# Kernel tuning notes

Hardware: AMD Instinct MI355X
Metric: run time of the kernel (lower is better)

## Reference

```python
import jax, jax.numpy as jnp
import numpy as np

B, N, T, C = 16, 12, 128, 128  # batch, num_classes (nodes), temporal, channels


def _bn(x, gamma, beta, eps=1e-5):
    # BatchNorm2d in training mode: stats over (batch, t, c), channel axis 1, biased var
    mean = jnp.mean(x, axis=(0, 2, 3), keepdims=True)
    var = jnp.var(x, axis=(0, 2, 3), keepdims=True)
    xn = (x - mean) * jax.lax.rsqrt(var + eps)
    return xn * gamma[None, :, None, None] + beta[None, :, None, None]


def setup_inputs() -> dict:
    key = jax.random.key(0)
    ks = jax.random.split(key, 3)
    scale = np.float32(np.sqrt(2.0 / C))
    inp = {
        'x': jax.random.normal(ks[0], (B, N, T, C), dtype=jnp.float32),
        'edge': jax.random.normal(ks[1], (B, N * N, T, C), dtype=jnp.float32),
    }
    wk = jax.random.split(ks[2], 10)
    for name, k in zip(['A1', 'B1', 'E1', 'U1', 'V1', 'A2', 'B2', 'E2', 'U2', 'V2'], wk):
        inp[name] = jax.random.normal(k, (C, C), dtype=jnp.float32) * scale
    for name, dim in [('g_e1', N * N), ('b_e1', N * N), ('g_v1', N), ('b_v1', N),
                      ('g_e2', N * N), ('b_e2', N * N), ('g_v2', N), ('b_v2', N)]:
        inp[name] = jnp.ones((dim,), jnp.float32) if name[0] == 'g' else jnp.zeros((dim,), jnp.float32)
    return inp


def _forward(x, edge, A1, B1, E1, U1, V1, A2, B2, E2, U2, V2,
             g_e1, b_e1, g_v1, b_v1, g_e2, b_e2, g_v2, b_v2):
    # create_e_matrix: edge index e = i*N + j; 'end' selects node i, 'start' selects node j.
    # Dense incidence einsums become pure gathers; the transpose einsum is a
    # scatter-add over j, i.e. a reshape + sum.
    i_idx = jnp.repeat(jnp.arange(N), N)  # end-node of each edge
    j_idx = jnp.tile(jnp.arange(N), N)    # start-node of each edge
    b, _, t, c = x.shape

    def layer(x, edge, A, Bw, E, U, V, ge, be, gv, bv, mask_node):
        res = x
        edge_upd = (x @ A.T)[:, i_idx] + (x @ Bw.T)[:, j_idx] + edge @ E.T
        edge_upd = _bn(edge_upd, ge, be)
        edge_upd = jnp.where(jnp.isnan(edge_upd), 0.0, edge_upd)
        edge = edge + jax.nn.relu(edge_upd)
        e = jax.nn.sigmoid(edge)
        e = jax.nn.softmax(e.reshape(b, N, N, t, c), axis=2).reshape(b, N * N, t, c)
        Ujx = (x @ V.T)[:, j_idx]
        agg = (e * Ujx).reshape(b, N, N, t, c).sum(axis=2) / N  # scatter to end nodes
        xn = _bn(x @ U.T + agg, gv, bv)
        if mask_node:  # original only NaN-masks node BN in layer 1
            xn = jnp.where(jnp.isnan(xn), 0.0, xn)
        return jax.nn.relu(res + xn), edge

    x, edge = layer(x, edge, A1, B1, E1, U1, V1, g_e1, b_e1, g_v1, b_v1, True)
    x, edge = layer(x, edge, A2, B2, E2, U2, V2, g_e2, b_e2, g_v2, b_v2, False)
    return x, edge


def reference(x, edge, A1, B1, E1, U1, V1, A2, B2, E2, U2, V2,
              g_e1, b_e1, g_v1, b_v1, g_e2, b_e2, g_v2, b_v2):
    return _forward(x, edge, A1, B1, E1, U1, V1, A2, B2, E2, U2, V2,
                    g_e1, b_e1, g_v1, b_v1, g_e2, b_e2, g_v2, b_v2)
```

## Files before the change

kernel.cpp:

```cpp
#include <hip/hip_runtime.h>
#include <hip/hip_bf16.h>

#define BB 16
#define NN 12
#define NE 144
#define TT 128
#define CC 128

typedef __attribute__((ext_vector_type(8))) short v8s;
typedef __attribute__((ext_vector_type(4))) short v4s;
typedef __attribute__((ext_vector_type(4))) float v4f;

__device__ __forceinline__ short f2bf(float f) {
    unsigned u = __float_as_uint(f);
    u += 0x7fffu + ((u >> 16) & 1u);
    return (short)(u >> 16);
}
__device__ __forceinline__ float bf2f(unsigned short u) {
    return __uint_as_float(((unsigned)u) << 16);
}
__device__ __forceinline__ float rndbf(float f) { return bf2f((unsigned short)f2bf(f)); }
__device__ __forceinline__ v4s f4_to_bf4(float4 a) {
    v4s r; r[0] = f2bf(a.x); r[1] = f2bf(a.y); r[2] = f2bf(a.z); r[3] = f2bf(a.w); return r;
}

__global__ __launch_bounds__(256) void kW(
    const float* A1, const float* B1, const float* E1, const float* U1, const float* V1,
    const float* A2, const float* B2, const float* E2, const float* U2, const float* V2,
    unsigned short* wb)
{
    int idx = blockIdx.x * 256 + threadIdx.x;
    int w = idx >> 14, r = idx & 16383;
    const float* s;
    switch (w) {
        case 0: s = A1; break; case 1: s = B1; break; case 2: s = E1; break;
        case 3: s = U1; break; case 4: s = V1; break; case 5: s = A2; break;
        case 6: s = B2; break; case 7: s = E2; break; case 8: s = U2; break;
        default: s = V2; break;
    }
    wb[idx] = (unsigned short)f2bf(s[r]);
}

__global__ __launch_bounds__(256) void kP(
    const float* __restrict__ x, const unsigned short* __restrict__ wb,
    int sA, int sB, int sV, int sU,
    unsigned short* __restrict__ oA, unsigned short* __restrict__ oB,
    unsigned short* __restrict__ oV, unsigned short* __restrict__ oU)
{
    __shared__ unsigned short xt[64][136];
    int tid = threadIdx.x;
    int m0 = blockIdx.x * 64;
    #pragma unroll
    for (int it = 0; it < 8; ++it) {
        int f = it * 256 + tid;
        int row = f >> 5, c4 = f & 31;
        float4 v = *reinterpret_cast<const float4*>(x + (size_t)m0 * 128 + (size_t)f * 4);
        *reinterpret_cast<v4s*>(&xt[row][c4 * 4]) = f4_to_bf4(v);
    }
    __syncthreads();
    int lane = tid & 63, wid = tid >> 6;
    int l15 = lane & 15, l4 = lane >> 4;

    const unsigned short* Ws[4] = { wb + (size_t)sA * 16384, wb + (size_t)sB * 16384,
                                    wb + (size_t)sV * 16384, wb + (size_t)sU * 16384 };
    unsigned short* Os[4] = { oA, oB, oV, oU };

    #pragma unroll
    for (int w = 0; w < 4; ++w) {
        const unsigned short* W = Ws[w];
        unsigned short* out = Os[w];
        v8s bfr[2][4];
        #pragma unroll
        for (int nt2 = 0; nt2 < 2; ++nt2) {
            int col = (wid * 2 + nt2) * 16 + l15;
            #pragma unroll
            for (int kk = 0; kk < 4; ++kk)
                bfr[nt2][kk] = *reinterpret_cast<const v8s*>(W + col * 128 + kk * 32 + l4 * 8);
        }
        v4f acc[4][2] = {};
        #pragma unroll
        for (int kk = 0; kk < 4; ++kk) {
            #pragma unroll
            for (int mt = 0; mt < 4; ++mt) {
                v8s a = *reinterpret_cast<const v8s*>(&xt[mt * 16 + l15][kk * 32 + l4 * 8]);
                acc[mt][0] = __builtin_amdgcn_mfma_f32_16x16x32_bf16(a, bfr[0][kk], acc[mt][0], 0, 0, 0);
                acc[mt][1] = __builtin_amdgcn_mfma_f32_16x16x32_bf16(a, bfr[1][kk], acc[mt][1], 0, 0, 0);
            }
        }
        #pragma unroll
        for (int mt = 0; mt < 4; ++mt) {
            #pragma unroll
            for (int nt2 = 0; nt2 < 2; ++nt2) {
                int col = (wid * 2 + nt2) * 16 + l15;
                #pragma unroll
                for (int reg = 0; reg < 4; ++reg) {
                    int rowg = m0 + mt * 16 + l4 * 4 + reg;
                    out[(size_t)rowg * 128 + col] = (unsigned short)f2bf(acc[mt][nt2][reg]);
                }
            }
        }
    }
}

template<bool IN_F32>
__global__ __launch_bounds__(256, 4) void kA(
    const float* __restrict__ ef32, const unsigned short* __restrict__ ebf_in,
    unsigned short* __restrict__ ebf_out,
    const unsigned short* __restrict__ xAp, const unsigned short* __restrict__ xBp,
    const unsigned short* __restrict__ Ebf, float2* __restrict__ epart)
{
    __shared__ unsigned short et[64][136];
    __shared__ float sblk[2];
    int tid = threadIdx.x;
    int bid = blockIdx.x;
    int th = bid & 1; int m = bid >> 1;
    int e = m % NE, b = m / NE;
    int iA = e / 12, jA = e - iA * 12;
    int t0 = th * 64;
    if (tid < 2) sblk[tid] = 0.f;
    size_t erow0 = ((size_t)(b * NE + e) * TT + t0) * CC;

    if constexpr (IN_F32) {
        #pragma unroll
        for (int it = 0; it < 8; ++it) {
            int f = it * 256 + tid;
            int row = f >> 5, c4 = f & 31;
            float4 v = *reinterpret_cast<const float4*>(ef32 + erow0 + (size_t)row * CC + c4 * 4);
            v4s bv = f4_to_bf4(v);
            *reinterpret_cast<v4s*>(&et[row][c4 * 4]) = bv;
            *reinterpret_cast<v4s*>(ebf_out + erow0 + (size_t)row * CC + c4 * 4) = bv;
        }
    } else {
        #pragma unroll
        for (int it = 0; it < 4; ++it) {
            int f = it * 256 + tid;
            int row = f >> 4, c8 = f & 15;
            *reinterpret_cast<v8s*>(&et[row][c8 * 8]) =
                *reinterpret_cast<const v8s*>(ebf_in + erow0 + (size_t)row * CC + c8 * 8);
        }
    }
    __syncthreads();

    int lane = tid & 63, wid = tid >> 6;
    int l15 = lane & 15, l4 = lane >> 4;

    v8s bfr[2][4];
    #pragma unroll
    for (int nt2 = 0; nt2 < 2; ++nt2) {
        int col = (wid * 2 + nt2) * 16 + l15;
        #pragma unroll
        for (int kk = 0; kk < 4; ++kk)
            bfr[nt2][kk] = *reinterpret_cast<const v8s*>(Ebf + col * 128 + kk * 32 + l4 * 8);
    }
    v4f acc[4][2] = {};
    #pragma unroll
    for (int kk = 0; kk < 4; ++kk) {
        #pragma unroll
        for (int mt = 0; mt < 4; ++mt) {
            v8s a = *reinterpret_cast<const v8s*>(&et[mt * 16 + l15][kk * 32 + l4 * 8]);
            acc[mt][0] = __builtin_amdgcn_mfma_f32_16x16x32_bf16(a, bfr[0][kk], acc[mt][0], 0, 0, 0);
            acc[mt][1] = __builtin_amdgcn_mfma_f32_16x16x32_bf16(a, bfr[1][kk], acc[mt][1], 0, 0, 0);
        }
    }
    __syncthreads();
    #pragma unroll
    for (int mt = 0; mt < 4; ++mt) {
        #pragma unroll
        for (int nt2 = 0; nt2 < 2; ++nt2) {
            int col = (wid * 2 + nt2) * 16 + l15;
            #pragma unroll
            for (int reg = 0; reg < 4; ++reg)
                et[mt * 16 + l4 * 4 + reg][col] = (unsigned short)f2bf(acc[mt][nt2][reg]);
        }
    }
    __syncthreads();
    size_t xaoff = ((size_t)(b * NN + iA) * TT + t0) * CC;
    size_t xboff = ((size_t)(b * NN + jA) * TT + t0) * CC;
    float s = 0.f, q = 0.f;
    #pragma unroll
    for (int it = 0; it < 4; ++it) {
        int f = it * 256 + tid;
        int row = f >> 4, c8 = f & 15;
        v8s ev = *reinterpret_cast<const v8s*>(&et[row][c8 * 8]);
        v8s xa = *reinterpret_cast<const v8s*>(xAp + xaoff + (size_t)row * CC + c8 * 8);
        v8s xb = *reinterpret_cast<const v8s*>(xBp + xboff + (size_t)row * CC + c8 * 8);
        #pragma unroll
        for (int k = 0; k < 8; ++k) {
            float v = bf2f((unsigned short)ev[k]) + bf2f((unsigned short)xa[k])
                    + bf2f((unsigned short)xb[k]);
            s += v; q += v * v;
        }
    }
    #pragma unroll
    for (int off = 1; off < 64; off <<= 1) { s += __shfl_xor(s, off); q += __shfl_xor(q, off); }
    if (lane == 0) { atomicAdd(&sblk[0], s); atomicAdd(&sblk[1], q); }
    __syncthreads();
    if (tid == 0) epart[bid] = make_float2(sblk[0], sblk[1]);
}

__global__ __launch_bounds__(64) void kRede(
    const float2* __restrict__ epart, const float* __restrict__ g,
    const float* __restrict__ be, float* __restrict__ estats)
{
    int e = blockIdx.x;
    int tid = threadIdx.x;
    float s = 0.f, q = 0.f;
    if (tid < 32) {
        int b = tid >> 1, th = tid & 1;
        float2 p = epart[(size_t)(b * NE + e) * 2 + th];
        s = p.x; q = p.y;
    }
    #pragma unroll
    for (int off = 1; off < 32; off <<= 1) { s += __shfl_xor(s, off); q += __shfl_xor(q, off); }
    if (tid == 0) {
        const float M = 262144.f;
        float mean = s / M;
        float var = q / M - mean * mean;
        float sc = g[e] * rsqrtf(var + 1e-5f);
        estats[e * 2] = sc;
        estats[e * 2 + 1] = be[e] - mean * sc;
    }
}

template<bool OUT_F32>
__global__ __launch_bounds__(256, 4) void kC(
    unsigned short* __restrict__ ebf,
    float* __restrict__ eout,
    const unsigned short* __restrict__ xAp, const unsigned short* __restrict__ xBp,
    const unsigned short* __restrict__ xV, const unsigned short* __restrict__ xU,
    const unsigned short* __restrict__ Ebf, const float* __restrict__ estats,
    unsigned short* __restrict__ yout, float* __restrict__ npart)
{
    __shared__ unsigned short et[48][136];
    __shared__ unsigned short xab[16][136];
    __shared__ unsigned short xv[12][136];
    __shared__ float2 scf[48];
    __shared__ float ns[4], nq[4];
    int tid = threadIdx.x;
    int bid = blockIdx.x;
    int third = bid % 3; int bt = bid / 3;
    int b = bt >> 7, t = bt & 127;
    if (tid < 48) scf[tid] = make_float2(estats[(third * 48 + tid) * 2],
                                         estats[(third * 48 + tid) * 2 + 1]);
    if (tid < 4) { ns[tid] = 0.f; nq[tid] = 0.f; }
    {
        int row = tid >> 4, c8 = tid & 15;
        const unsigned short* src = (row < 4)
            ? (xAp + (((size_t)(b * NN + third * 4 + row) * TT) + t) * CC)
            : (xBp + (((size_t)(b * NN + (row - 4)) * TT) + t) * CC);
        *reinterpret_cast<v8s*>(&xab[row][c8 * 8]) = *reinterpret_cast<const v8s*>(src + c8 * 8);
    }
    if (tid < 192) {
        int row = tid >> 4, c8 = tid & 15;
        *reinterpret_cast<v8s*>(&xv[row][c8 * 8]) =
            *reinterpret_cast<const v8s*>(xV + (((size_t)(b * NN + row) * TT) + t) * CC + c8 * 8);
    }
    #pragma unroll
    for (int it = 0; it < 3; ++it) {
        int f = it * 256 + tid;
        int row = f >> 4, c8 = f & 15;
        *reinterpret_cast<v8s*>(&et[row][c8 * 8]) =
            *reinterpret_cast<const v8s*>(ebf + (((size_t)(b * NE + third * 48 + row) * TT) + t) * CC + c8 * 8);
    }
    __syncthreads();
    int lane = tid & 63, wid = tid >> 6;
    int l15 = lane & 15, l4 = lane >> 4;

    v8s bfr[2][4];
    #pragma unroll
    for (int nt2 = 0; nt2 < 2; ++nt2) {
        int col = (wid * 2 + nt2) * 16 + l15;
        #pragma unroll
        for (int kk = 0; kk < 4; ++kk)
            bfr[nt2][kk] = *reinterpret_cast<const v8s*>(Ebf + col * 128 + kk * 32 + l4 * 8);
    }
    v4f acc[3][2] = {};
    #pragma unroll
    for (int kk = 0; kk < 4; ++kk) {
        #pragma unroll
        for (int mt = 0; mt < 3; ++mt) {
            v8s a = *reinterpret_cast<const v8s*>(&et[mt * 16 + l15][kk * 32 + l4 * 8]);
            acc[mt][0] = __builtin_amdgcn_mfma_f32_16x16x32_bf16(a, bfr[0][kk], acc[mt][0], 0, 0, 0);
            acc[mt][1] = __builtin_amdgcn_mfma_f32_16x16x32_bf16(a, bfr[1][kk], acc[mt][1], 0, 0, 0);
        }
    }
    __syncthreads();
    #pragma unroll
    for (int mt = 0; mt < 3; ++mt) {
        #pragma unroll
        for (int reg = 0; reg < 4; ++reg) {
            int r = mt * 16 + l4 * 4 + reg;
            int il = r / 12, jl = r - il * 12;
            float2 sc = scf[r];
            #pragma unroll
            for (int nt2 = 0; nt2 < 2; ++nt2) {
                int col = (wid * 2 + nt2) * 16 + l15;
                float upd = rndbf(acc[mt][nt2][reg]) + bf2f(xab[il][col]) + bf2f(xab[4 + jl][col]);
                float bn = fmaxf(sc.x * upd + sc.y, 0.f);
                float en = bf2f(et[r][col]) + bn;
                et[r][col] = (unsigned short)f2bf(en);
                if constexpr (OUT_F32) {
                    int eg = third * 48 + r;
                    eout[(((size_t)(b * NE + eg) * TT) + t) * CC + col] = en;
                }
            }
        }
    }
    __syncthreads();
    if constexpr (!OUT_F32) {
        #pragma unroll
        for (int it = 0; it < 3; ++it) {
            int f = it * 256 + tid;
            int row = f >> 4, c8 = f & 15;
            *reinterpret_cast<v8s*>(ebf + (((size_t)(b * NE + third * 48 + row) * TT) + t) * CC + c8 * 8) =
                *reinterpret_cast<const v8s*>(&et[row][c8 * 8]);
        }
    }
    #pragma unroll
    for (int ph = 0; ph < 2; ++ph) {
        int u = tid + ph * 256;
        int il = u >> 7, c = u & 127;
        float den = 0.f, ag = 0.f;
        #pragma unroll
        for (int j = 0; j < 12; ++j) {
            float sv = bf2f(et[il * 12 + j][c]);
            float sg = 1.f / (1.f + __expf(-sv));
            float ev = __expf(sg);
            den += ev;
            ag += ev * bf2f(xv[j][c]);
        }
        float agg = ag / (den * 12.f);
        int i = third * 4 + il;
        size_t xa = (((size_t)(b * NN + i) * TT) + t) * CC + c;
        float yv = bf2f(xU[xa]) + agg;
        unsigned short us = (unsigned short)f2bf(yv);
        yout[xa] = us;
        float yr = bf2f(us);
        float s1 = yr, s2 = yr * yr;
        #pragma unroll
        for (int off = 1; off < 64; off <<= 1) { s1 += __shfl_xor(s1, off); s2 += __shfl_xor(s2, off); }
        if (lane == 0) { atomicAdd(&ns[il], s1); atomicAdd(&nq[il], s2); }
    }
    __syncthreads();
    if (tid < 4) {
        npart[(size_t)bid * 8 + tid * 2 + 0] = ns[tid];
        npart[(size_t)bid * 8 + tid * 2 + 1] = nq[tid];
    }
}

__global__ __launch_bounds__(256) void kRedn(
    const float* __restrict__ npart, const float* __restrict__ g,
    const float* __restrict__ be, float* __restrict__ nstats)
{
    int n = blockIdx.x;
    int third = n >> 2, il = n & 3;
    float s = 0.f, q = 0.f;
    for (int bt = threadIdx.x; bt < 2048; bt += 256) {
        const float* p = npart + ((size_t)(bt * 3 + third) * 8 + il * 2);
        s += p[0]; q += p[1];
    }
    __shared__ float ss[4], qq[4];
    #pragma unroll
    for (int off = 32; off >= 1; off >>= 1) { s += __shfl_down(s, off); q += __shfl_down(q, off); }
    int wid = threadIdx.x >> 6;
    if ((threadIdx.x & 63) == 0) { ss[wid] = s; qq[wid] = q; }
    __syncthreads();
    if (threadIdx.x == 0) {
        s = ss[0] + ss[1] + ss[2] + ss[3];
        q = qq[0] + qq[1] + qq[2] + qq[3];
        const float M = 262144.f;
        float mean = s / M;
        float var = q / M - mean * mean;
        float sc = g[n] * rsqrtf(var + 1e-5f);
        nstats[n * 2] = sc;
        nstats[n * 2 + 1] = be[n] - mean * sc;
    }
}

__global__ __launch_bounds__(256) void kE(
    const float* xres, const unsigned short* __restrict__ yin,
    const float* __restrict__ nstats, float* xout)
{
    int idx4 = blockIdx.x * 256 + threadIdx.x;
    size_t base = (size_t)idx4 * 4;
    int n = (int)((base >> 14) % 12);
    float scv = nstats[n * 2], shv = nstats[n * 2 + 1];
    float4 xvv = *reinterpret_cast<const float4*>(xres + base);
    v4s yv4 = *reinterpret_cast<const v4s*>(yin + base);
    float4 o;
    o.x = fmaxf(xvv.x + scv * bf2f((unsigned short)yv4[0]) + shv, 0.f);
    o.y = fmaxf(xvv.y + scv * bf2f((unsigned short)yv4[1]) + shv, 0.f);
    o.z = fmaxf(xvv.z + scv * bf2f((unsigned short)yv4[2]) + shv, 0.f);
    o.w = fmaxf(xvv.w + scv * bf2f((unsigned short)yv4[3]) + shv, 0.f);
    *reinterpret_cast<float4*>(xout + base) = o;
}

extern "C" void kernel_launch(void* const* d_in, const int* in_sizes, int n_in,
                              void* d_out, int out_size, void* d_ws, size_t ws_size,
                              hipStream_t stream)
{
    const float* x0 = (const float*)d_in[0];
    const float* e0 = (const float*)d_in[1];
    const float* W[10];
    for (int i = 0; i < 10; ++i) W[i] = (const float*)d_in[2 + i];
    const float* ge1 = (const float*)d_in[12];
    const float* be1 = (const float*)d_in[13];
    const float* gv1 = (const float*)d_in[14];
    const float* bv1 = (const float*)d_in[15];
    const float* ge2 = (const float*)d_in[16];
    const float* be2 = (const float*)d_in[17];
    const float* gv2 = (const float*)d_in[18];
    const float* bv2 = (const float*)d_in[19];

    const size_t SZX = (size_t)BB * NN * TT * CC;
    const size_t SZE = (size_t)BB * NE * TT * CC;
    float* out_x = (float*)d_out;
    float* out_e = out_x + SZX;

    unsigned short* ws16 = (unsigned short*)d_ws;
    unsigned short* xA = ws16;
    unsigned short* xB = ws16 + SZX;
    unsigned short* xV = ws16 + 2 * SZX;
    unsigned short* xU = ws16 + 3 * SZX;
    unsigned short* yb = ws16 + 4 * SZX;
    unsigned short* ebf = ws16 + 5 * SZX;
    float2* epart  = (float2*)(ebf + SZE);
    float* estats = (float*)(epart + 4608);
    float* npart  = estats + 288;
    float* nstats = npart + 49152;
    unsigned short* wb = (unsigned short*)(nstats + 24);

    float* x1 = out_x;

    kW<<<640, 256, 0, stream>>>(W[0], W[1], W[2], W[3], W[4], W[5], W[6], W[7], W[8], W[9], wb);

    kP<<<384, 256, 0, stream>>>(x0, wb, 0, 1, 4, 3, xA, xB, xV, xU);
    kA<true><<<4608, 256, 0, stream>>>(e0, nullptr, ebf, xA, xB, wb + 2 * 16384, epart);
    kRede<<<144, 64, 0, stream>>>(epart, ge1, be1, estats);
    kC<false><<<6144, 256, 0, stream>>>(ebf, nullptr, xA, xB, xV, xU,
                                        wb + 2 * 16384, estats, yb, npart);
    kRedn<<<12, 256, 0, stream>>>(npart, gv1, bv1, nstats);
    kE<<<3072, 256, 0, stream>>>(x0, yb, nstats, x1);

    kP<<<384, 256, 0, stream>>>(x1, wb, 5, 6, 9, 8, xA, xB, xV, xU);
    kA<false><<<4608, 256, 0, stream>>>(nullptr, ebf, nullptr, xA, xB, wb + 7 * 16384, epart);
    kRede<<<144, 64, 0, stream>>>(epart, ge2, be2, estats);
    kC<true><<<6144, 256, 0, stream>>>(ebf, out_e, xA, xB, xV, xU,
                                       wb + 7 * 16384, estats, yb, npart);
    kRedn<<<12, 256, 0, stream>>>(npart, gv2, bv2, nstats);
    kE<<<3072, 256, 0, stream>>>(x1, yb, nstats, out_x);
}
```

Measured before the change: 274.9 us.

## Split kA into quarter-time tiles and fold edge BN stats reduction into kC

kA now handles 32 time steps per block instead of 64, which doubles the grid and raises the occupancy hint. The separate kRede kernel is removed. Each kC block instead reduces the per-block partial sums for its 48 edges and builds the BN scale and shift itself. The f32 edge output in kC is also written with coalesced vectorized float4 stores from shared memory instead of scattered scalar stores. The cost is redundant stats reduction across the 6144 kC blocks (each reads 64 partials per edge), in exchange for one fewer launch per layer.

```diff
diff --git a/kernel.cpp b/kernel.cpp
--- a/kernel.cpp
+++ b/kernel.cpp
@@ -103,26 +103,26 @@
 }
 
 template<bool IN_F32>
-__global__ __launch_bounds__(256, 4) void kA(
+__global__ __launch_bounds__(256, 6) void kA(
     const float* __restrict__ ef32, const unsigned short* __restrict__ ebf_in,
     unsigned short* __restrict__ ebf_out,
     const unsigned short* __restrict__ xAp, const unsigned short* __restrict__ xBp,
     const unsigned short* __restrict__ Ebf, float2* __restrict__ epart)
 {
-    __shared__ unsigned short et[64][136];
+    __shared__ unsigned short et[32][136];
     __shared__ float sblk[2];
     int tid = threadIdx.x;
     int bid = blockIdx.x;
-    int th = bid & 1; int m = bid >> 1;
+    int th = bid & 3; int m = bid >> 2;
     int e = m % NE, b = m / NE;
     int iA = e / 12, jA = e - iA * 12;
-    int t0 = th * 64;
+    int t0 = th * 32;
     if (tid < 2) sblk[tid] = 0.f;
     size_t erow0 = ((size_t)(b * NE + e) * TT + t0) * CC;
 
     if constexpr (IN_F32) {
         #pragma unroll
-        for (int it = 0; it < 8; ++it) {
+        for (int it = 0; it < 4; ++it) {
             int f = it * 256 + tid;
             int row = f >> 5, c4 = f & 31;
             float4 v = *reinterpret_cast<const float4*>(ef32 + erow0 + (size_t)row * CC + c4 * 4);
@@ -132,7 +132,7 @@
         }
     } else {
         #pragma unroll
-        for (int it = 0; it < 4; ++it) {
+        for (int it = 0; it < 2; ++it) {
             int f = it * 256 + tid;
             int row = f >> 4, c8 = f & 15;
             *reinterpret_cast<v8s*>(&et[row][c8 * 8]) =
@@ -152,11 +152,11 @@
         for (int kk = 0; kk < 4; ++kk)
             bfr[nt2][kk] = *reinterpret_cast<const v8s*>(Ebf + col * 128 + kk * 32 + l4 * 8);
     }
-    v4f acc[4][2] = {};
+    v4f acc[2][2] = {};
     #pragma unroll
     for (int kk = 0; kk < 4; ++kk) {
         #pragma unroll
-        for (int mt = 0; mt < 4; ++mt) {
+        for (int mt = 0; mt < 2; ++mt) {
             v8s a = *reinterpret_cast<const v8s*>(&et[mt * 16 + l15][kk * 32 + l4 * 8]);
             acc[mt][0] = __builtin_amdgcn_mfma_f32_16x16x32_bf16(a, bfr[0][kk], acc[mt][0], 0, 0, 0);
             acc[mt][1] = __builtin_amdgcn_mfma_f32_16x16x32_bf16(a, bfr[1][kk], acc[mt][1], 0, 0, 0);
@@ -164,7 +164,7 @@
     }
     __syncthreads();
     #pragma unroll
-    for (int mt = 0; mt < 4; ++mt) {
+    for (int mt = 0; mt < 2; ++mt) {
         #pragma unroll
         for (int nt2 = 0; nt2 < 2; ++nt2) {
             int col = (wid * 2 + nt2) * 16 + l15;
@@ -178,7 +178,7 @@
     size_t xboff = ((size_t)(b * NN + jA) * TT + t0) * CC;
     float s = 0.f, q = 0.f;
     #pragma unroll
-    for (int it = 0; it < 4; ++it) {
+    for (int it = 0; it < 2; ++it) {
         int f = it * 256 + tid;
         int row = f >> 4, c8 = f & 15;
         v8s ev = *reinterpret_cast<const v8s*>(&et[row][c8 * 8]);
@@ -198,37 +198,15 @@
     if (tid == 0) epart[bid] = make_float2(sblk[0], sblk[1]);
 }
 
-__global__ __launch_bounds__(64) void kRede(
-    const float2* __restrict__ epart, const float* __restrict__ g,
-    const float* __restrict__ be, float* __restrict__ estats)
-{
-    int e = blockIdx.x;
-    int tid = threadIdx.x;
-    float s = 0.f, q = 0.f;
-    if (tid < 32) {
-        int b = tid >> 1, th = tid & 1;
-        float2 p = epart[(size_t)(b * NE + e) * 2 + th];
-        s = p.x; q = p.y;
-    }
-    #pragma unroll
-    for (int off = 1; off < 32; off <<= 1) { s += __shfl_xor(s, off); q += __shfl_xor(q, off); }
-    if (tid == 0) {
-        const float M = 262144.f;
-        float mean = s / M;
-        float var = q / M - mean * mean;
-        float sc = g[e] * rsqrtf(var + 1e-5f);
-        estats[e * 2] = sc;
-        estats[e * 2 + 1] = be[e] - mean * sc;
-    }
-}
-
 template<bool OUT_F32>
-__global__ __launch_bounds__(256, 4) void kC(
+__global__ __launch_bounds__(256, 5) void kC(
     unsigned short* __restrict__ ebf,
     float* __restrict__ eout,
     const unsigned short* __restrict__ xAp, const unsigned short* __restrict__ xBp,
     const unsigned short* __restrict__ xV, const unsigned short* __restrict__ xU,
-    const unsigned short* __restrict__ Ebf, const float* __restrict__ estats,
+    const unsigned short* __restrict__ Ebf,
+    const float2* __restrict__ epart, const float* __restrict__ gw,
+    const float* __restrict__ bw,
     unsigned short* __restrict__ yout, float* __restrict__ npart)
 {
     __shared__ unsigned short et[48][136];
@@ -240,9 +218,26 @@
     int bid = blockIdx.x;
     int third = bid % 3; int bt = bid / 3;
     int b = bt >> 7, t = bt & 127;
-    if (tid < 48) scf[tid] = make_float2(estats[(third * 48 + tid) * 2],
-                                         estats[(third * 48 + tid) * 2 + 1]);
     if (tid < 4) { ns[tid] = 0.f; nq[tid] = 0.f; }
+    if (tid < 192) {
+        int r = tid >> 2, part = tid & 3;
+        int eg = third * 48 + r;
+        float s0 = 0.f, q0 = 0.f;
+        #pragma unroll
+        for (int b2 = 0; b2 < 16; ++b2) {
+            float2 p = epart[(size_t)(b2 * NE + eg) * 4 + part];
+            s0 += p.x; q0 += p.y;
+        }
+        s0 += __shfl_xor(s0, 1); q0 += __shfl_xor(q0, 1);
+        s0 += __shfl_xor(s0, 2); q0 += __shfl_xor(q0, 2);
+        if (part == 0) {
+            const float M = 262144.f;
+            float mean = s0 / M;
+            float var = q0 / M - mean * mean;
+            float sc = gw[eg] * rsqrtf(var + 1e-5f);
+            scf[r] = make_float2(sc, bw[eg] - mean * sc);
+        }
+    }
     {
         int row = tid >> 4, c8 = tid & 15;
         const unsigned short* src = (row < 4)
@@ -299,21 +294,26 @@
                 float bn = fmaxf(sc.x * upd + sc.y, 0.f);
                 float en = bf2f(et[r][col]) + bn;
                 et[r][col] = (unsigned short)f2bf(en);
-                if constexpr (OUT_F32) {
-                    int eg = third * 48 + r;
-                    eout[(((size_t)(b * NE + eg) * TT) + t) * CC + col] = en;
-                }
             }
         }
     }
     __syncthreads();
-    if constexpr (!OUT_F32) {
-        #pragma unroll
-        for (int it = 0; it < 3; ++it) {
-            int f = it * 256 + tid;
-            int row = f >> 4, c8 = f & 15;
-            *reinterpret_cast<v8s*>(ebf + (((size_t)(b * NE + third * 48 + row) * TT) + t) * CC + c8 * 8) =
-                *reinterpret_cast<const v8s*>(&et[row][c8 * 8]);
+    #pragma unroll
+    for (int it = 0; it < 3; ++it) {
+        int f = it * 256 + tid;
+        int row = f >> 4, c8 = f & 15;
+        size_t goff = (((size_t)(b * NE + third * 48 + row) * TT) + t) * CC + c8 * 8;
+        v8s nv = *reinterpret_cast<const v8s*>(&et[row][c8 * 8]);
+        if constexpr (OUT_F32) {
+            float4 o0, o1;
+            o0.x = bf2f((unsigned short)nv[0]); o0.y = bf2f((unsigned short)nv[1]);
+            o0.z = bf2f((unsigned short)nv[2]); o0.w = bf2f((unsigned short)nv[3]);
+            o1.x = bf2f((unsigned short)nv[4]); o1.y = bf2f((unsigned short)nv[5]);
+            o1.z = bf2f((unsigned short)nv[6]); o1.w = bf2f((unsigned short)nv[7]);
+            *reinterpret_cast<float4*>(eout + goff)     = o0;
+            *reinterpret_cast<float4*>(eout + goff + 4) = o1;
+        } else {
+            *reinterpret_cast<v8s*>(ebf + goff) = nv;
         }
     }
     #pragma unroll
@@ -425,8 +425,7 @@
     unsigned short* yb = ws16 + 4 * SZX;
     unsigned short* ebf = ws16 + 5 * SZX;
     float2* epart  = (float2*)(ebf + SZE);
-    float* estats = (float*)(epart + 4608);
-    float* npart  = estats + 288;
+    float* npart  = (float*)(epart + 9216);
     float* nstats = npart + 49152;
     unsigned short* wb = (unsigned short*)(nstats + 24);
 
@@ -435,18 +434,16 @@
     kW<<<640, 256, 0, stream>>>(W[0], W[1], W[2], W[3], W[4], W[5], W[6], W[7], W[8], W[9], wb);
 
     kP<<<384, 256, 0, stream>>>(x0, wb, 0, 1, 4, 3, xA, xB, xV, xU);
-    kA<true><<<4608, 256, 0, stream>>>(e0, nullptr, ebf, xA, xB, wb + 2 * 16384, epart);
-    kRede<<<144, 64, 0, stream>>>(epart, ge1, be1, estats);
+    kA<true><<<9216, 256, 0, stream>>>(e0, nullptr, ebf, xA, xB, wb + 2 * 16384, epart);
     kC<false><<<6144, 256, 0, stream>>>(ebf, nullptr, xA, xB, xV, xU,
-                                        wb + 2 * 16384, estats, yb, npart);
+                                        wb + 2 * 16384, epart, ge1, be1, yb, npart);
     kRedn<<<12, 256, 0, stream>>>(npart, gv1, bv1, nstats);
     kE<<<3072, 256, 0, stream>>>(x0, yb, nstats, x1);
 
     kP<<<384, 256, 0, stream>>>(x1, wb, 5, 6, 9, 8, xA, xB, xV, xU);
-    kA<false><<<4608, 256, 0, stream>>>(nullptr, ebf, nullptr, xA, xB, wb + 7 * 16384, epart);
-    kRede<<<144, 64, 0, stream>>>(epart, ge2, be2, estats);
+    kA<false><<<9216, 256, 0, stream>>>(nullptr, ebf, nullptr, xA, xB, wb + 7 * 16384, epart);
     kC<true><<<6144, 256, 0, stream>>>(ebf, out_e, xA, xB, xV, xU,
-                                       wb + 7 * 16384, estats, yb, npart);
+                                       wb + 7 * 16384, epart, ge2, be2, yb, npart);
     kRedn<<<12, 256, 0, stream>>>(npart, gv2, bv2, nstats);
     kE<<<3072, 256, 0, stream>>>(x1, yb, nstats, out_x);
 }
```

Result: slower. 307.5 us (+11.8%).
